# Optimization experiments

Measured on AMD Instinct MI355X. Metric: run time of the kernel, lower is better.

The kernel has to match this reference:

```python
import jax, jax.numpy as jnp
import numpy as np

N_HEADS = 16

def setup_inputs() -> dict:
    key = jax.random.key(0)
    ks = jax.random.split(key, 5)
    D = 2048
    x = jax.random.normal(ks[0], (2, 2048, D), dtype=jnp.float32)
    scale = 1.0 / np.sqrt(D)
    Wq = jax.random.normal(ks[1], (D, D), dtype=jnp.float32) * scale
    Wk = jax.random.normal(ks[2], (D, D), dtype=jnp.float32) * scale
    Wv = jax.random.normal(ks[3], (D, D), dtype=jnp.float32) * scale
    Wo = jax.random.normal(ks[4], (D, D), dtype=jnp.float32) * scale
    return {"x": x, "Wq": Wq, "Wk": Wk, "Wv": Wv, "Wo": Wo}


def reference(x, Wq, Wk, Wv, Wo):
    # Causal multi-head attention. The original module computes it one query
    # position at a time (recompute loop) but the math is standard causal MHA:
    # query pos attends to key positions 0..pos.
    B, S, D = x.shape
    H = N_HEADS
    hd = D // H
    def split_heads(t):
        return t.reshape(B, S, H, hd).transpose(0, 2, 1, 3)  # (B,H,S,hd)
    q = split_heads(x @ Wq.T)
    k = split_heads(x @ Wk.T)
    v = split_heads(x @ Wv.T)
    scores = jnp.einsum('bhqd,bhkd->bhqk', q, k) / jnp.sqrt(jnp.asarray(hd, x.dtype))
    causal = jnp.tril(jnp.ones((S, S), dtype=bool))  # (S,S), True where allowed
    scores = jnp.where(causal[None, None], scores, jnp.asarray(-jnp.inf, scores.dtype))
    attn = jax.nn.softmax(scores, axis=-1)
    out = jnp.einsum('bhqk,bhkd->bhqd', attn, v)
    out = out.transpose(0, 2, 1, 3).reshape(B, S, D)
    return out @ Wo.T
```

## Files before the change

kernel.cpp:

```cpp
#include <hip/hip_runtime.h>
#include <hip/hip_bf16.h>
#include <stdint.h>

#define DD 2048
#define SS 2048
#define NB 2
#define NH 16
#define HDIM 128
#define MM (NB*SS)

typedef __attribute__((ext_vector_type(8))) short bf16x8;
typedef __attribute__((ext_vector_type(4))) float f32x4;
typedef __attribute__((ext_vector_type(4))) ushort u16x4;

__device__ __forceinline__ float fast_exp2(float x) {
  return __builtin_amdgcn_exp2f(x);
}

__device__ __forceinline__ ushort f2bf(float f) {
  union { __hip_bfloat16 h; ushort u; } v;
  v.h = __float2bfloat16(f);
  return v.u;
}

__device__ __forceinline__ void gld_lds16(const ushort* g, ushort* l) {
  __builtin_amdgcn_global_load_lds(
      (const __attribute__((address_space(1))) void*)g,
      (__attribute__((address_space(3))) void*)l, 16, 0, 0);
}

__global__ __launch_bounds__(256) void cvt_all(
    const float* __restrict__ x, const float* __restrict__ wq,
    const float* __restrict__ wk, const float* __restrict__ wv,
    const float* __restrict__ wo, ushort* __restrict__ dst)
{
  const int X8 = MM * DD / 8;
  const int W8 = DD * DD / 8;
  const int TOT8 = X8 + 4*W8;
  for (int i8 = blockIdx.x * 256 + threadIdx.x; i8 < TOT8;
       i8 += gridDim.x * 256) {
    const float* src; int off;
    if (i8 < X8)            { src = x;  off = i8; }
    else if (i8 < X8 +   W8){ src = wq; off = i8 - X8; }
    else if (i8 < X8 + 2*W8){ src = wk; off = i8 - (X8 +   W8); }
    else if (i8 < X8 + 3*W8){ src = wv; off = i8 - (X8 + 2*W8); }
    else                    { src = wo; off = i8 - (X8 + 3*W8); }
    const float4* p = (const float4*)src;
    float4 a = p[(long)off*2], b = p[(long)off*2 + 1];
    bf16x8 o;
    o[0]=(short)f2bf(a.x); o[1]=(short)f2bf(a.y); o[2]=(short)f2bf(a.z); o[3]=(short)f2bf(a.w);
    o[4]=(short)f2bf(b.x); o[5]=(short)f2bf(b.y); o[6]=(short)f2bf(b.z); o[7]=(short)f2bf(b.w);
    *(bf16x8*)(dst + (long)i8*8) = o;
  }
}

__global__ __launch_bounds__(256, 2) void gemm_qkv(
    const ushort* __restrict__ A, const ushort* __restrict__ Bt,
    ushort* __restrict__ Qo, ushort* __restrict__ Ko, ushort* __restrict__ Vt)
{
  __shared__ ushort lds[3 * 12288];
  const int t = threadIdx.x;
  const int bid = blockIdx.x;
  const int xcd = bid & 7, local = bid >> 3;
  const int NBX = 6;
  const int bm = local / NBX;
  const int bn = xcd * NBX + (local - bm * NBX);
  const int lane = t & 63, w = t >> 6;
  const int wr = w >> 1, wcn = w & 1;
  const int lr = lane & 15, lg = lane >> 4;

  int aoff[4], boff[2];
#pragma unroll
  for (int i = 0; i < 4; ++i) {
    int p = i*256 + t, ln = p >> 3, sr = (p & 7) ^ (ln & 7);
    aoff[i] = (2*ln + (sr >> 2)) * DD + (sr & 3) * 8;
  }
#pragma unroll
  for (int i = 0; i < 2; ++i) {
    int p = i*256 + t, ln = p >> 3, sr = (p & 7) ^ (ln & 7);
    boff[i] = (2*ln + (sr >> 2)) * DD + (sr & 3) * 8;
  }
  const ushort* Ab = A  + (long)(bm*256) * DD;
  const ushort* Bb = Bt + (long)(bn*128) * DD;

#define STG_A01(KT, BUF) do { const ushort* g_ = Ab + (KT)*32;             \
    ushort* l_ = lds + (BUF)*12288;                                        \
    gld_lds16(g_ + aoff[0], l_ + t*8);                                     \
    gld_lds16(g_ + aoff[1], l_ + (256 + t)*8); } while (0)
#define STG_A23(KT, BUF) do { const ushort* g_ = Ab + (KT)*32;             \
    ushort* l_ = lds + (BUF)*12288;                                        \
    gld_lds16(g_ + aoff[2], l_ + (512 + t)*8);                             \
    gld_lds16(g_ + aoff[3], l_ + (768 + t)*8); } while (0)
#define STG_B(KT, BUF)   do { const ushort* g_ = Bb + (KT)*32;             \
    ushort* l_ = lds + (BUF)*12288 + 8192;                                 \
    gld_lds16(g_ + boff[0], l_ + t*8);                                     \
    gld_lds16(g_ + boff[1], l_ + (256 + t)*8); } while (0)
#define LDA(dst, m) { int r_ = wr*128 + (m)*16 + lr; int ln_ = r_ >> 1;    \
    int sl_ = (lg + ((r_ & 1) << 2)) ^ (ln_ & 7);                          \
    (dst) = *(const bf16x8*)(cb + ln_*128 + sl_*16); }
#define LDB(dst, n) { int r_ = wcn*64 + (n)*16 + lr; int ln_ = r_ >> 1;    \
    int sl_ = (lg + ((r_ & 1) << 2)) ^ (ln_ & 7);                          \
    (dst) = *(const bf16x8*)(cb + 16384 + ln_*128 + sl_*16); }
#define MFMA42(AV, BV, MB, NB_) do {                                       \
    __builtin_amdgcn_s_setprio(1);                                         \
    _Pragma("unroll") for (int m = 0; m < 4; ++m)                          \
    _Pragma("unroll") for (int n = 0; n < 2; ++n)                          \
      acc[(MB)+m][(NB_)+n] = __builtin_amdgcn_mfma_f32_16x16x32_bf16(      \
          AV[m], BV[n], acc[(MB)+m][(NB_)+n], 0, 0, 0);                    \
    __builtin_amdgcn_s_setprio(0); } while (0)
#define SB  __builtin_amdgcn_sched_barrier(0)
#define BAR __builtin_amdgcn_s_barrier()
#define LGKM0 asm volatile("s_waitcnt lgkmcnt(0)" ::: "memory")

  f32x4 acc[8][4] = {};
  const int T = DD / 32;

  STG_A01(0, 0); STG_A23(0, 0); STG_B(0, 0);
  STG_A01(1, 1); STG_A23(1, 1); STG_B(1, 1);
  asm volatile("s_waitcnt vmcnt(6)" ::: "memory");
  SB; BAR; SB;

  for (int kt = 0; kt < T; ++kt) {
    const char* cb = (const char*)lds + (kt % 3) * 24576;
    const int bs = (kt + 2) % 3;
    const bool st = (kt + 2 < T);
    bf16x8 a03[4], a47[4], b01[2], b23[2];
    LDA(a03[0],0); LDA(a03[1],1); LDA(a03[2],2); LDA(a03[3],3);
    LDB(b01[0],0); LDB(b01[1],1);
    if (st) STG_A01(kt+2, bs);
    SB; BAR; LGKM0; SB;
    MFMA42(a03, b01, 0, 0);
    SB; BAR; SB;
    LDA(a47[0],4); LDA(a47[1],5); LDA(a47[2],6); LDA(a47[3],7);
    if (st) STG_A23(kt+2, bs);
    SB; BAR; LGKM0; SB;
    MFMA42(a47, b01, 4, 0);
    SB; BAR; SB;
    LDB(b23[0],2); LDB(b23[1],3);
    if (st) STG_B(kt+2, bs);
    SB; BAR; LGKM0; SB;
    MFMA42(a03, b23, 0, 2);
    SB; BAR; SB;
    if (st)              { asm volatile("s_waitcnt vmcnt(6)" ::: "memory"); }
    else if (kt + 1 < T) { asm volatile("s_waitcnt vmcnt(0)" ::: "memory"); }
    SB; BAR; SB;
    MFMA42(a47, b23, 4, 2);
    SB; BAR; SB;
  }
#undef STG_A01
#undef STG_A23
#undef STG_B
#undef LDA
#undef LDB
#undef MFMA42

  const int crb = bm*256 + wr*128 + lg*4;
  const int region = bn >> 4;
  const int ccb = (bn & 15)*128 + wcn*64 + lr;
  if (region < 2) {
    const float scale = (region == 0) ? (0.08838834764831845f * 1.4426950408889634f) : 1.0f;
    ushort* C = (region == 0) ? Qo : Ko;
#pragma unroll
    for (int m = 0; m < 8; ++m)
#pragma unroll
      for (int n = 0; n < 4; ++n)
#pragma unroll
        for (int j = 0; j < 4; ++j)
          C[(long)(crb + m*16 + j) * DD + (ccb + n*16)] = f2bf(acc[m][n][j] * scale);
  } else {
#pragma unroll
    for (int m = 0; m < 8; ++m) {
      int sg = crb + m*16;
      int b2 = sg >> 11, s2 = sg & 2047;
#pragma unroll
      for (int n = 0; n < 4; ++n) {
        int colv = ccb + n*16;
        int h2 = colv >> 7, d2 = colv & 127;
        u16x4 pk;
        pk[0] = f2bf(acc[m][n][0]); pk[1] = f2bf(acc[m][n][1]);
        pk[2] = f2bf(acc[m][n][2]); pk[3] = f2bf(acc[m][n][3]);
        *(u16x4*)(Vt + ((long)((b2*NH + h2)*HDIM + d2)) * SS + s2) = pk;
      }
    }
  }
#undef SB
#undef BAR
#undef LGKM0
}

__global__ __launch_bounds__(256, 3) void gemm_o128(
    const ushort* __restrict__ A, const ushort* __restrict__ Bt,
    float* __restrict__ Cf)
{
  __shared__ ushort lds[3 * 8192];
  const int t = threadIdx.x;
  const int bid = blockIdx.x;
  const int xcd = bid & 7, local = bid >> 3;
  const int bm = local >> 1;
  const int bn = xcd * 2 + (local & 1);
  const int lane = t & 63, w = t >> 6;
  const int wr = w >> 1, wcn = w & 1;
  const int lr = lane & 15, lg = lane >> 4;

  int aoff[2], boff[2];
#pragma unroll
  for (int i = 0; i < 2; ++i) {
    int p = i*256 + t, ln = p >> 3, sr = (p & 7) ^ (ln & 7);
    aoff[i] = (2*ln + (sr >> 2)) * DD + (sr & 3) * 8;
    boff[i] = aoff[i];
  }
  const ushort* Ab = A  + (long)(bm*128) * DD;
  const ushort* Bb = Bt + (long)(bn*128) * DD;

#define STG_A(KT, BUF) do { const ushort* g_ = Ab + (KT)*32;               \
    ushort* l_ = lds + (BUF)*8192;                                         \
    gld_lds16(g_ + aoff[0], l_ + t*8);                                     \
    gld_lds16(g_ + aoff[1], l_ + (256 + t)*8); } while (0)
#define STG_B(KT, BUF) do { const ushort* g_ = Bb + (KT)*32;               \
    ushort* l_ = lds + (BUF)*8192 + 4096;                                  \
    gld_lds16(g_ + boff[0], l_ + t*8);                                     \
    gld_lds16(g_ + boff[1], l_ + (256 + t)*8); } while (0)
#define LDA(dst, m) { int r_ = wr*64 + (m)*16 + lr; int ln_ = r_ >> 1;     \
    int sl_ = (lg + ((r_ & 1) << 2)) ^ (ln_ & 7);                          \
    (dst) = *(const bf16x8*)(cb + ln_*128 + sl_*16); }
#define LDB(dst, n) { int r_ = wcn*64 + (n)*16 + lr; int ln_ = r_ >> 1;    \
    int sl_ = (lg + ((r_ & 1) << 2)) ^ (ln_ & 7);                          \
    (dst) = *(const bf16x8*)(cb + 8192 + ln_*128 + sl_*16); }
#define MFMA8(AV, BV, NB_) do {                                            \
    __builtin_amdgcn_s_setprio(1);                                         \
    _Pragma("unroll") for (int m = 0; m < 4; ++m)                          \
    _Pragma("unroll") for (int n = 0; n < 2; ++n)                          \
      acc[m][(NB_)+n] = __builtin_amdgcn_mfma_f32_16x16x32_bf16(           \
          AV[m], BV[n], acc[m][(NB_)+n], 0, 0, 0);                         \
    __builtin_amdgcn_s_setprio(0); } while (0)
#define SB  __builtin_amdgcn_sched_barrier(0)
#define BAR __builtin_amdgcn_s_barrier()
#define LGKM0 asm volatile("s_waitcnt lgkmcnt(0)" ::: "memory")

  f32x4 acc[4][4] = {};
  const int T = DD / 32;

  STG_A(0, 0); STG_B(0, 0);
  STG_A(1, 1); STG_B(1, 1);
  asm volatile("s_waitcnt vmcnt(4)" ::: "memory");
  SB; BAR; SB;

  for (int kt = 0; kt < T; ++kt) {
    const char* cb = (const char*)lds + (kt % 3) * 16384;
    const int bs = (kt + 2) % 3;
    const bool st = (kt + 2 < T);
    bf16x8 a[4], b01[2], b23[2];
    LDA(a[0],0); LDA(a[1],1); LDA(a[2],2); LDA(a[3],3);
    LDB(b01[0],0); LDB(b01[1],1);
    if (st) STG_A(kt+2, bs);
    SB; BAR; LGKM0; SB;
    MFMA8(a, b01, 0);
    SB; BAR; SB;
    LDB(b23[0],2); LDB(b23[1],3);
    if (st) STG_B(kt+2, bs);
    SB; BAR; LGKM0; SB;
    MFMA8(a, b23, 2);
    SB;
    if (st)              { asm volatile("s_waitcnt vmcnt(4)" ::: "memory"); }
    else if (kt + 1 < T) { asm volatile("s_waitcnt vmcnt(0)" ::: "memory"); }
    SB; BAR; SB;
  }
#undef STG_A
#undef STG_B
#undef LDA
#undef LDB
#undef MFMA8
#undef SB
#undef BAR
#undef LGKM0

  const int crb = bm*128 + wr*64 + lg*4;
  const int ccb = bn*128 + wcn*64 + lr;
#pragma unroll
  for (int m = 0; m < 4; ++m)
#pragma unroll
    for (int n = 0; n < 4; ++n)
#pragma unroll
      for (int j = 0; j < 4; ++j)
        Cf[(long)(crb + m*16 + j) * DD + (ccb + n*16)] = acc[m][n][j];
}

__global__ __launch_bounds__(512, 2) void attn_fwd(
    const ushort* __restrict__ Qb, const ushort* __restrict__ Kb,
    const ushort* __restrict__ Vtg, ushort* __restrict__ Ob)
{
  __shared__ ushort Ks[2][128*128];
  __shared__ ushort Vs[2][128*128];
  __shared__ ushort Ps[8*16*68];

  const int bid = blockIdx.x;
  const int p = bid >> 5;
  const int bh = bid & 31;
  const int b = bh >> 4, h = bh & 15;
  const int t = threadIdx.x;
  const int lane = t & 63;
  const int wq = t >> 6;
  const int lr = lane & 15, lg = lane >> 4;

  bf16x8 ones;
#pragma unroll
  for (int i = 0; i < 8; ++i) ones[i] = (short)0x3F80;

  int koff[4], voff[4];
#pragma unroll
  for (int i = 0; i < 4; ++i) {
    int c = i*512 + t;
    int kr = c >> 4, kc = c & 15;
    koff[i] = kr*DD + ((kc ^ (kr & 7)) * 8);
    voff[i] = kr*SS + ((kc ^ (kr & 7)) * 8);
  }
  const ushort* Kg = Kb + (long)(b * SS) * DD + h * HDIM;
  const ushort* Vg = Vtg + (long)(bh * HDIM) * SS;

#define STAGE(KT, BUF) do {                                     \
    const ushort* kg_ = Kg + (long)(KT) * 128 * DD;             \
    const ushort* vg_ = Vg + (KT) * 128;                        \
    _Pragma("unroll") for (int i_ = 0; i_ < 4; ++i_) {          \
      gld_lds16(kg_ + koff[i_], &Ks[BUF][i_*4096 + t*8]);       \
      gld_lds16(vg_ + voff[i_], &Vs[BUF][i_*4096 + t*8]);       \
    } } while (0)

  ushort* myP = Ps + wq * (16*68);
  const int n0 = p + 1;
  const int TOT = 17;

  STAGE(0, 0);
  __syncthreads();

  int u = 0;
  for (int half = 0; half < 2; ++half) {
    const int qt = half ? (15 - p) : p;
    const int qbase = qt * 128;
    const long rowQ = (long)(b * SS + qbase + wq * 16);
    const int ntile = qt + 1;
    const int qminw = qbase + wq*16;

    bf16x8 qf[4];
#pragma unroll
    for (int c = 0; c < 4; ++c)
      qf[c] = *(const bf16x8*)(Qb + (rowQ + lr) * DD + h*HDIM + c*32 + lg*8);

    f32x4 accO[8] = {};
    f32x4 accL = {};
    float mrow[4];
#pragma unroll
    for (int j = 0; j < 4; ++j) mrow[j] = -1e30f;

    for (int kt = 0; kt < ntile; ++kt, ++u) {
      const int k0 = kt * 128;
      const int cur = u & 1;
      if (u + 1 < TOT) {
        const int un = u + 1;
        const int ktn = (un < n0) ? un : un - n0;
        STAGE(ktn, cur ^ 1);
      }

      const ushort* Kc = Ks[cur];
      const ushort* Vc = Vs[cur];
      f32x4 sc[8] = {};
      __builtin_amdgcn_s_setprio(1);
#pragma unroll
      for (int n = 0; n < 8; ++n) {
        int r = n*16 + lr;
        int swz = (r & 7) << 4;
#pragma unroll
        for (int c = 0; c < 4; ++c) {
          bf16x8 kf = *(const bf16x8*)((const char*)Kc + ((r*256 + c*64 + lg*16) ^ swz));
          sc[n] = __builtin_amdgcn_mfma_f32_16x16x32_bf16(qf[c], kf, sc[n], 0,0,0);
        }
      }
      __builtin_amdgcn_s_setprio(0);
      if (kt == ntile - 1) {
#pragma unroll
        for (int n = 0; n < 8; ++n)
#pragma unroll
          for (int j = 0; j < 4; ++j) {
            int kpos = k0 + n*16 + lr;
            int qpos = qminw + lg*4 + j;
            if (kpos > qpos) sc[n][j] = -1e30f;
          }
      }
      float tm[4]; float gd = -1e30f;
#pragma unroll
      for (int j = 0; j < 4; ++j) {
        float m8 = fmaxf(fmaxf(fmaxf(sc[0][j], sc[1][j]), fmaxf(sc[2][j], sc[3][j])),
                         fmaxf(fmaxf(sc[4][j], sc[5][j]), fmaxf(sc[6][j], sc[7][j])));
#pragma unroll
        for (int off = 1; off < 16; off <<= 1) m8 = fmaxf(m8, __shfl_xor(m8, off));
        tm[j] = m8;
        gd = fmaxf(gd, m8 - mrow[j]);
      }
      const bool resc = !__all(gd <= 8.0f);
      if (resc) {
        float al[4];
#pragma unroll
        for (int j = 0; j < 4; ++j) {
          float mn = fmaxf(mrow[j], tm[j]);
          al[j] = fast_exp2(mrow[j] - mn);
          mrow[j] = mn;
        }
#pragma unroll
        for (int dg = 0; dg < 8; ++dg) {
          f32x4 v = accO[dg];
          v[0] *= al[0]; v[1] *= al[1]; v[2] *= al[2]; v[3] *= al[3];
          accO[dg] = v;
        }
        accL[0] *= al[0]; accL[1] *= al[1]; accL[2] *= al[2]; accL[3] *= al[3];
      }
#pragma unroll
      for (int j = 0; j < 4; ++j)
#pragma unroll
        for (int n = 0; n < 8; ++n)
          sc[n][j] = fast_exp2(sc[n][j] - mrow[j]);
#pragma unroll
      for (int hh = 0; hh < 2; ++hh) {
#pragma unroll
        for (int n2 = 0; n2 < 4; ++n2)
#pragma unroll
          for (int j = 0; j < 4; ++j)
            myP[(lg*4 + j)*68 + n2*16 + lr] = f2bf(sc[hh*4 + n2][j]);
        bf16x8 pa0 = *(const bf16x8*)(myP + lr*68 + lg*8);
        bf16x8 pa1 = *(const bf16x8*)(myP + lr*68 + 32 + lg*8);
        __builtin_amdgcn_s_setprio(1);
        accL = __builtin_amdgcn_mfma_f32_16x16x32_bf16(pa0, ones, accL, 0,0,0);
        accL = __builtin_amdgcn_mfma_f32_16x16x32_bf16(pa1, ones, accL, 0,0,0);
#pragma unroll
        for (int dg = 0; dg < 8; ++dg) {
          int d = dg*16 + lr;
          int vswz = (d & 7) << 4;
          bf16x8 v0 = *(const bf16x8*)((const char*)Vc + ((d*256 + hh*128 + lg*16) ^ vswz));
          bf16x8 v1 = *(const bf16x8*)((const char*)Vc + ((d*256 + hh*128 + 64 + lg*16) ^ vswz));
          accO[dg] = __builtin_amdgcn_mfma_f32_16x16x32_bf16(pa0, v0, accO[dg], 0,0,0);
          accO[dg] = __builtin_amdgcn_mfma_f32_16x16x32_bf16(pa1, v1, accO[dg], 0,0,0);
        }
        __builtin_amdgcn_s_setprio(0);
      }
      __syncthreads();
    }

    float inv[4];
#pragma unroll
    for (int j = 0; j < 4; ++j) inv[j] = 1.0f / accL[j];
    ushort* Og = Ob + rowQ * DD + h * HDIM;
#pragma unroll
    for (int dg = 0; dg < 8; ++dg)
#pragma unroll
      for (int j = 0; j < 4; ++j)
        Og[(long)(lg*4 + j) * DD + dg*16 + lr] = f2bf(accO[dg][j] * inv[j]);
  }
#undef STAGE
}

extern "C" void kernel_launch(void* const* d_in, const int* in_sizes, int n_in,
                              void* d_out, int out_size, void* d_ws, size_t ws_size,
                              hipStream_t stream) {
  const float* x  = (const float*)d_in[0];
  const float* Wq = (const float*)d_in[1];
  const float* Wk = (const float*)d_in[2];
  const float* Wv = (const float*)d_in[3];
  const float* Wo = (const float*)d_in[4];

  ushort* ws  = (ushort*)d_ws;
  ushort* xb  = ws;
  ushort* wqb = ws  + (long)MM*DD;
  ushort* wkb = wqb + (long)DD*DD;
  ushort* wvb = wkb + (long)DD*DD;
  ushort* wob = wvb + (long)DD*DD;
  ushort* Qb  = wob + (long)DD*DD;
  ushort* Kb  = Qb  + (long)MM*DD;
  ushort* Vtg = Kb  + (long)MM*DD;
  (void)wkb; (void)wvb;

  cvt_all<<<2048, 256, 0, stream>>>(x, Wq, Wk, Wv, Wo, ws);

  gemm_qkv<<<768, 256, 0, stream>>>(xb, wqb, Qb, Kb, Vtg);

  attn_fwd<<<256, 512, 0, stream>>>(Qb, Kb, Vtg, xb);

  gemm_o128<<<512, 256, 0, stream>>>(xb, wob, (float*)d_out);
}
```

Baseline: 244.2 us.

## Give each attention wave 32 query rows with 4 waves per block

The attention kernel now runs 4 waves of 256 threads instead of 8 waves, and each wave handles two 16-row query sub-tiles. Every K and V fragment read from LDS then feeds two MFMAs, which halves LDS fragment traffic per unit of compute. The cost is roughly double the accumulator and score registers per wave, fewer waves available to hide latency, and twice as many global-to-LDS staging loads per thread.

```diff
diff --git a/kernel.cpp b/kernel.cpp
--- a/kernel.cpp
+++ b/kernel.cpp
@@ -285,13 +285,13 @@
         Cf[(long)(crb + m*16 + j) * DD + (ccb + n*16)] = acc[m][n][j];
 }
 
-__global__ __launch_bounds__(512, 2) void attn_fwd(
+__global__ __launch_bounds__(256, 2) void attn_fwd(
     const ushort* __restrict__ Qb, const ushort* __restrict__ Kb,
     const ushort* __restrict__ Vtg, ushort* __restrict__ Ob)
 {
   __shared__ ushort Ks[2][128*128];
   __shared__ ushort Vs[2][128*128];
-  __shared__ ushort Ps[8*16*68];
+  __shared__ ushort Ps[4*32*68];
 
   const int bid = blockIdx.x;
   const int p = bid >> 5;
@@ -306,10 +306,10 @@
 #pragma unroll
   for (int i = 0; i < 8; ++i) ones[i] = (short)0x3F80;
 
-  int koff[4], voff[4];
-#pragma unroll
-  for (int i = 0; i < 4; ++i) {
-    int c = i*512 + t;
+  int koff[8], voff[8];
+#pragma unroll
+  for (int i = 0; i < 8; ++i) {
+    int c = i*256 + t;
     int kr = c >> 4, kc = c & 15;
     koff[i] = kr*DD + ((kc ^ (kr & 7)) * 8);
     voff[i] = kr*SS + ((kc ^ (kr & 7)) * 8);
@@ -320,12 +320,12 @@
 #define STAGE(KT, BUF) do {                                     \
     const ushort* kg_ = Kg + (long)(KT) * 128 * DD;             \
     const ushort* vg_ = Vg + (KT) * 128;                        \
-    _Pragma("unroll") for (int i_ = 0; i_ < 4; ++i_) {          \
-      gld_lds16(kg_ + koff[i_], &Ks[BUF][i_*4096 + t*8]);       \
-      gld_lds16(vg_ + voff[i_], &Vs[BUF][i_*4096 + t*8]);       \
+    _Pragma("unroll") for (int i_ = 0; i_ < 8; ++i_) {          \
+      gld_lds16(kg_ + koff[i_], &Ks[BUF][i_*2048 + t*8]);       \
+      gld_lds16(vg_ + voff[i_], &Vs[BUF][i_*2048 + t*8]);       \
     } } while (0)
 
-  ushort* myP = Ps + wq * (16*68);
+  ushort* myP = Ps + wq * (32*68);
   const int n0 = p + 1;
   const int TOT = 17;
 
@@ -336,20 +336,24 @@
   for (int half = 0; half < 2; ++half) {
     const int qt = half ? (15 - p) : p;
     const int qbase = qt * 128;
-    const long rowQ = (long)(b * SS + qbase + wq * 16);
+    const long rowQ = (long)(b * SS + qbase + wq * 32);
     const int ntile = qt + 1;
-    const int qminw = qbase + wq*16;
-
-    bf16x8 qf[4];
-#pragma unroll
-    for (int c = 0; c < 4; ++c)
-      qf[c] = *(const bf16x8*)(Qb + (rowQ + lr) * DD + h*HDIM + c*32 + lg*8);
-
-    f32x4 accO[8] = {};
-    f32x4 accL = {};
-    float mrow[4];
-#pragma unroll
-    for (int j = 0; j < 4; ++j) mrow[j] = -1e30f;
+    const int qminw = qbase + wq*32;
+
+    bf16x8 qf[2][4];
+#pragma unroll
+    for (int i = 0; i < 2; ++i)
+#pragma unroll
+      for (int c = 0; c < 4; ++c)
+        qf[i][c] = *(const bf16x8*)(Qb + (rowQ + i*16 + lr) * DD + h*HDIM + c*32 + lg*8);
+
+    f32x4 accO[2][8] = {};
+    f32x4 accL[2] = {};
+    float mrow[2][4];
+#pragma unroll
+    for (int i = 0; i < 2; ++i)
+#pragma unroll
+      for (int j = 0; j < 4; ++j) mrow[i][j] = -1e30f;
 
     for (int kt = 0; kt < ntile; ++kt, ++u) {
       const int k0 = kt * 128;
@@ -362,7 +366,7 @@
 
       const ushort* Kc = Ks[cur];
       const ushort* Vc = Vs[cur];
-      f32x4 sc[8] = {};
+      f32x4 sc[2][8] = {};
       __builtin_amdgcn_s_setprio(1);
 #pragma unroll
       for (int n = 0; n < 8; ++n) {
@@ -371,87 +375,113 @@
 #pragma unroll
         for (int c = 0; c < 4; ++c) {
           bf16x8 kf = *(const bf16x8*)((const char*)Kc + ((r*256 + c*64 + lg*16) ^ swz));
-          sc[n] = __builtin_amdgcn_mfma_f32_16x16x32_bf16(qf[c], kf, sc[n], 0,0,0);
+          sc[0][n] = __builtin_amdgcn_mfma_f32_16x16x32_bf16(qf[0][c], kf, sc[0][n], 0,0,0);
+          sc[1][n] = __builtin_amdgcn_mfma_f32_16x16x32_bf16(qf[1][c], kf, sc[1][n], 0,0,0);
         }
       }
       __builtin_amdgcn_s_setprio(0);
       if (kt == ntile - 1) {
 #pragma unroll
-        for (int n = 0; n < 8; ++n)
-#pragma unroll
-          for (int j = 0; j < 4; ++j) {
-            int kpos = k0 + n*16 + lr;
-            int qpos = qminw + lg*4 + j;
-            if (kpos > qpos) sc[n][j] = -1e30f;
-          }
+        for (int i = 0; i < 2; ++i)
+#pragma unroll
+          for (int n = 0; n < 8; ++n)
+#pragma unroll
+            for (int j = 0; j < 4; ++j) {
+              int kpos = k0 + n*16 + lr;
+              int qpos = qminw + i*16 + lg*4 + j;
+              if (kpos > qpos) sc[i][n][j] = -1e30f;
+            }
       }
-      float tm[4]; float gd = -1e30f;
-#pragma unroll
-      for (int j = 0; j < 4; ++j) {
-        float m8 = fmaxf(fmaxf(fmaxf(sc[0][j], sc[1][j]), fmaxf(sc[2][j], sc[3][j])),
-                         fmaxf(fmaxf(sc[4][j], sc[5][j]), fmaxf(sc[6][j], sc[7][j])));
-#pragma unroll
-        for (int off = 1; off < 16; off <<= 1) m8 = fmaxf(m8, __shfl_xor(m8, off));
-        tm[j] = m8;
-        gd = fmaxf(gd, m8 - mrow[j]);
-      }
+      float tm[2][4]; float gd = -1e30f;
+#pragma unroll
+      for (int i = 0; i < 2; ++i)
+#pragma unroll
+        for (int j = 0; j < 4; ++j) {
+          float m8 = fmaxf(fmaxf(fmaxf(sc[i][0][j], sc[i][1][j]), fmaxf(sc[i][2][j], sc[i][3][j])),
+                           fmaxf(fmaxf(sc[i][4][j], sc[i][5][j]), fmaxf(sc[i][6][j], sc[i][7][j])));
+#pragma unroll
+          for (int off = 1; off < 16; off <<= 1) m8 = fmaxf(m8, __shfl_xor(m8, off));
+          tm[i][j] = m8;
+          gd = fmaxf(gd, m8 - mrow[i][j]);
+        }
       const bool resc = !__all(gd <= 8.0f);
       if (resc) {
-        float al[4];
-#pragma unroll
-        for (int j = 0; j < 4; ++j) {
-          float mn = fmaxf(mrow[j], tm[j]);
-          al[j] = fast_exp2(mrow[j] - mn);
-          mrow[j] = mn;
+        float al[2][4];
+#pragma unroll
+        for (int i = 0; i < 2; ++i)
+#pragma unroll
+          for (int j = 0; j < 4; ++j) {
+            float mn = fmaxf(mrow[i][j], tm[i][j]);
+            al[i][j] = fast_exp2(mrow[i][j] - mn);
+            mrow[i][j] = mn;
+          }
+#pragma unroll
+        for (int i = 0; i < 2; ++i) {
+#pragma unroll
+          for (int dg = 0; dg < 8; ++dg) {
+            f32x4 v = accO[i][dg];
+            v[0] *= al[i][0]; v[1] *= al[i][1]; v[2] *= al[i][2]; v[3] *= al[i][3];
+            accO[i][dg] = v;
+          }
+          accL[i][0] *= al[i][0]; accL[i][1] *= al[i][1];
+          accL[i][2] *= al[i][2]; accL[i][3] *= al[i][3];
         }
-#pragma unroll
-        for (int dg = 0; dg < 8; ++dg) {
-          f32x4 v = accO[dg];
-          v[0] *= al[0]; v[1] *= al[1]; v[2] *= al[2]; v[3] *= al[3];
-          accO[dg] = v;
-        }
-        accL[0] *= al[0]; accL[1] *= al[1]; accL[2] *= al[2]; accL[3] *= al[3];
       }
 #pragma unroll
-      for (int j = 0; j < 4; ++j)
-#pragma unroll
-        for (int n = 0; n < 8; ++n)
-          sc[n][j] = fast_exp2(sc[n][j] - mrow[j]);
+      for (int i = 0; i < 2; ++i)
+#pragma unroll
+        for (int j = 0; j < 4; ++j)
+#pragma unroll
+          for (int n = 0; n < 8; ++n)
+            sc[i][n][j] = fast_exp2(sc[i][n][j] - mrow[i][j]);
 #pragma unroll
       for (int hh = 0; hh < 2; ++hh) {
 #pragma unroll
-        for (int n2 = 0; n2 < 4; ++n2)
-#pragma unroll
-          for (int j = 0; j < 4; ++j)
-            myP[(lg*4 + j)*68 + n2*16 + lr] = f2bf(sc[hh*4 + n2][j]);
-        bf16x8 pa0 = *(const bf16x8*)(myP + lr*68 + lg*8);
-        bf16x8 pa1 = *(const bf16x8*)(myP + lr*68 + 32 + lg*8);
+        for (int i = 0; i < 2; ++i)
+#pragma unroll
+          for (int n2 = 0; n2 < 4; ++n2)
+#pragma unroll
+            for (int j = 0; j < 4; ++j)
+              myP[(i*16 + lg*4 + j)*68 + n2*16 + lr] = f2bf(sc[i][hh*4 + n2][j]);
+        bf16x8 pa[2][2];
+#pragma unroll
+        for (int i = 0; i < 2; ++i)
+#pragma unroll
+          for (int kc = 0; kc < 2; ++kc)
+            pa[i][kc] = *(const bf16x8*)(myP + (i*16 + lr)*68 + kc*32 + lg*8);
         __builtin_amdgcn_s_setprio(1);
-        accL = __builtin_amdgcn_mfma_f32_16x16x32_bf16(pa0, ones, accL, 0,0,0);
-        accL = __builtin_amdgcn_mfma_f32_16x16x32_bf16(pa1, ones, accL, 0,0,0);
+        accL[0] = __builtin_amdgcn_mfma_f32_16x16x32_bf16(pa[0][0], ones, accL[0], 0,0,0);
+        accL[0] = __builtin_amdgcn_mfma_f32_16x16x32_bf16(pa[0][1], ones, accL[0], 0,0,0);
+        accL[1] = __builtin_amdgcn_mfma_f32_16x16x32_bf16(pa[1][0], ones, accL[1], 0,0,0);
+        accL[1] = __builtin_amdgcn_mfma_f32_16x16x32_bf16(pa[1][1], ones, accL[1], 0,0,0);
 #pragma unroll
         for (int dg = 0; dg < 8; ++dg) {
           int d = dg*16 + lr;
           int vswz = (d & 7) << 4;
           bf16x8 v0 = *(const bf16x8*)((const char*)Vc + ((d*256 + hh*128 + lg*16) ^ vswz));
           bf16x8 v1 = *(const bf16x8*)((const char*)Vc + ((d*256 + hh*128 + 64 + lg*16) ^ vswz));
-          accO[dg] = __builtin_amdgcn_mfma_f32_16x16x32_bf16(pa0, v0, accO[dg], 0,0,0);
-          accO[dg] = __builtin_amdgcn_mfma_f32_16x16x32_bf16(pa1, v1, accO[dg], 0,0,0);
+          accO[0][dg] = __builtin_amdgcn_mfma_f32_16x16x32_bf16(pa[0][0], v0, accO[0][dg], 0,0,0);
+          accO[0][dg] = __builtin_amdgcn_mfma_f32_16x16x32_bf16(pa[0][1], v1, accO[0][dg], 0,0,0);
+          accO[1][dg] = __builtin_amdgcn_mfma_f32_16x16x32_bf16(pa[1][0], v0, accO[1][dg], 0,0,0);
+          accO[1][dg] = __builtin_amdgcn_mfma_f32_16x16x32_bf16(pa[1][1], v1, accO[1][dg], 0,0,0);
         }
         __builtin_amdgcn_s_setprio(0);
       }
       __syncthreads();
     }
 
-    float inv[4];
-#pragma unroll
-    for (int j = 0; j < 4; ++j) inv[j] = 1.0f / accL[j];
     ushort* Og = Ob + rowQ * DD + h * HDIM;
 #pragma unroll
-    for (int dg = 0; dg < 8; ++dg)
-#pragma unroll
-      for (int j = 0; j < 4; ++j)
-        Og[(long)(lg*4 + j) * DD + dg*16 + lr] = f2bf(accO[dg][j] * inv[j]);
+    for (int i = 0; i < 2; ++i) {
+      float inv[4];
+#pragma unroll
+      for (int j = 0; j < 4; ++j) inv[j] = 1.0f / accL[i][j];
+#pragma unroll
+      for (int dg = 0; dg < 8; ++dg)
+#pragma unroll
+        for (int j = 0; j < 4; ++j)
+          Og[(long)(i*16 + lg*4 + j) * DD + dg*16 + lr] = f2bf(accO[i][dg][j] * inv[j]);
+    }
   }
 #undef STAGE
 }
@@ -480,7 +510,7 @@
 
   gemm_qkv<<<768, 256, 0, stream>>>(xb, wqb, Qb, Kb, Vtg);
 
-  attn_fwd<<<256, 512, 0, stream>>>(Qb, Kb, Vtg, xb);
+  attn_fwd<<<256, 256, 0, stream>>>(Qb, Kb, Vtg, xb);
 
   gemm_o128<<<512, 256, 0, stream>>>(xb, wob, (float*)d_out);
 }
```

New measurement: 265.6 us. +8.8%, slower.
